# Performance work log

Hardware: AMD Instinct MI355X
Metric: run time of the kernel (lower is better)

## Reference

```python
import jax, jax.numpy as jnp
import numpy as np

B, D_IN, D_OUT, N_DISJOINT = 4096, 256, 256, 64


def setup_inputs() -> dict:
    key = jax.random.key(0)
    k_x, k_sel, k_w, k_b = jax.random.split(key, 4)
    x = jax.random.normal(k_x, (B, D_IN), dtype=jnp.float32)
    sel_idx = jax.random.randint(k_sel, (B,), 0, N_DISJOINT)
    one_hot_selector = jax.nn.one_hot(sel_idx, N_DISJOINT, dtype=jnp.float32)
    # torch nn.Linear default init: U(-1/sqrt(fan_in), 1/sqrt(fan_in)), fan_in = num_disjoint
    bound = 1.0 / np.sqrt(N_DISJOINT)
    # W[d] is the [in, out] weight matrix for disjoint block d
    W = jax.random.uniform(k_w, (N_DISJOINT, D_IN, D_OUT), dtype=jnp.float32, minval=-bound, maxval=bound)
    Bw = jax.random.uniform(k_b, (N_DISJOINT, D_OUT), dtype=jnp.float32, minval=-bound, maxval=bound)
    return {"x": x, "one_hot_selector": one_hot_selector, "W": W, "Bw": Bw}


def reference(x, one_hot_selector, W, Bw):
    # Same math as: w = (selector @ weights.T).view(B, in, out); h = einsum('bij,bi->bj', w, x)
    # Reordered contraction avoids the [B, in, out] intermediate:
    v = jnp.einsum('bi,dio->bdo', x, W)          # [B, D, out]
    h = jnp.einsum('bd,bdo->bo', one_hot_selector, v)  # [B, out]
    bias = one_hot_selector @ Bw                  # [B, out]
    return h + bias
```

## Files before the change

kernel.cpp:

```cpp
#include <hip/hip_runtime.h>


#define NBLK 64
#define BCAP 1024
#define BCAPX 256
#define CPAD 16

typedef __attribute__((ext_vector_type(8))) short bf16x8;
typedef __attribute__((ext_vector_type(4))) float f32x4;

__device__ __forceinline__ unsigned short f2bf(float f) {
    unsigned u = __float_as_uint(f);
    u += 0x7FFFu + ((u >> 16) & 1u);
    return (unsigned short)(u >> 16);
}

__global__ __launch_bounds__(256) void dd_prep(
    const float* __restrict__ x,
    const float* __restrict__ onehot,
    int* __restrict__ counts,
    int* __restrict__ buckets,
    unsigned short* __restrict__ xbs)
{
    __shared__ int rowd[32];
    __shared__ int gslot[32];
    __shared__ int lhist[NBLK];
    __shared__ int lbase[NBLK];
    const int t = threadIdx.x;
    const int w = t >> 6;
    const int lane = t & 63;
    if (t < NBLK) lhist[t] = 0;

    const int row0 = blockIdx.x * 32;
#pragma unroll
    for (int i = 0; i < 8; ++i) {
        const int row = row0 + w * 8 + i;
        const float v = onehot[(size_t)row * NBLK + lane];
        const unsigned long long mm = __ballot(v > 0.5f);
        const int dd = (int)__ffsll(mm) - 1;
        if (lane == 0) rowd[w * 8 + i] = dd;
    }
    ushort4 bv[8];
#pragma unroll
    for (int i = 0; i < 8; ++i) {
        const int row = row0 + w * 8 + i;
        const float4 v = ((const float4*)(x + ((size_t)row << 8)))[lane];
        bv[i].x = f2bf(v.x); bv[i].y = f2bf(v.y);
        bv[i].z = f2bf(v.z); bv[i].w = f2bf(v.w);
    }
    __syncthreads();

    int d = 0, slot = 0;
    if (t < 32) {
        d = rowd[t];
        slot = atomicAdd(&lhist[d], 1);
    }
    __syncthreads();
    if (t < NBLK && lhist[t] > 0)
        lbase[t] = atomicAdd(&counts[t * CPAD], lhist[t]);
    __syncthreads();
    if (t < 32) {
        const int g = lbase[d] + slot;
        gslot[t] = g;
        if (g < BCAP) buckets[d * BCAP + g] = row0 + t;
    }
    __syncthreads();
#pragma unroll
    for (int i = 0; i < 8; ++i) {
        const int idx = w * 8 + i;
        const int gd  = rowd[idx];
        const int g   = gslot[idx];
        if (g < BCAPX)
            *(ushort4*)(xbs + ((size_t)(gd * BCAPX + g) << 8) + lane * 4) = bv[i];
    }
}

__global__ __launch_bounds__(256) void dd_compute(
    const unsigned short* __restrict__ xbs,
    const float* __restrict__ W,
    const float* __restrict__ Bw,
    const int* __restrict__ counts,
    const int* __restrict__ buckets,
    float* __restrict__ out)
{
    const int t    = threadIdx.x;
    const int lane = t & 63;
    const int w    = t >> 6;
    const int d    = blockIdx.x & 63;
    const int task = blockIdx.x >> 6;
    const int rt   = task >> 2;
    const int ct   = task & 3;
    const int cw   = ct * 64 + w * 16;
    const int m    = lane & 15;
    const int qd   = lane >> 4;

    int cnt = counts[d * CPAD];
    cnt = cnt < BCAPX ? cnt : BCAPX;
    if (rt * 32 >= cnt) return;

    const float* wb = W + ((size_t)d << 16) + (size_t)(qd * 8) * 256 + (cw + m);
    bf16x8 bfrag[8];
#pragma unroll
    for (int kb = 0; kb < 8; ++kb) {
        const float* wp = wb + (size_t)(kb * 32) * 256;
#pragma unroll
        for (int j = 0; j < 8; ++j)
            bfrag[kb][j] = (short)f2bf(wp[j * 256]);
    }

    const float bias = Bw[d * 256 + cw + m];
    const int* bkt = buckets + d * BCAP;
    const unsigned short* xd = xbs + ((size_t)(d * BCAPX) << 8);

    for (int base = rt * 32; base < cnt; base += 128) {
        const int i0 = base + m;
        const int i1 = base + 16 + m;
        const int ic0 = i0 < cnt ? i0 : cnt - 1;
        const int ic1 = i1 < cnt ? i1 : cnt - 1;
        const unsigned short* xp0 = xd + ((size_t)ic0 << 8) + qd * 8;
        const unsigned short* xp1 = xd + ((size_t)ic1 << 8) + qd * 8;

        int rid0[4], rid1[4];
#pragma unroll
        for (int reg = 0; reg < 4; ++reg) {
            const int rl0 = base + qd * 4 + reg;
            const int rl1 = base + 16 + qd * 4 + reg;
            rid0[reg] = bkt[rl0 < cnt ? rl0 : cnt - 1];
            rid1[reg] = bkt[rl1 < cnt ? rl1 : cnt - 1];
        }

        f32x4 acc0 = {bias, bias, bias, bias};
        f32x4 acc1 = {bias, bias, bias, bias};
#pragma unroll
        for (int kb = 0; kb < 8; ++kb) {
            bf16x8 a0 = *(const bf16x8*)(xp0 + kb * 32);
            acc0 = __builtin_amdgcn_mfma_f32_16x16x32_bf16(a0, bfrag[kb], acc0, 0, 0, 0);
        }
#pragma unroll
        for (int kb = 0; kb < 8; ++kb) {
            bf16x8 a1 = *(const bf16x8*)(xp1 + kb * 32);
            acc1 = __builtin_amdgcn_mfma_f32_16x16x32_bf16(a1, bfrag[kb], acc1, 0, 0, 0);
        }

#pragma unroll
        for (int reg = 0; reg < 4; ++reg) {
            const int rl0 = base + qd * 4 + reg;
            if (rl0 < cnt) out[((size_t)rid0[reg] << 8) + cw + m] = acc0[reg];
            const int rl1 = base + 16 + qd * 4 + reg;
            if (rl1 < cnt) out[((size_t)rid1[reg] << 8) + cw + m] = acc1[reg];
        }
    }
}

extern "C" void kernel_launch(void* const* d_in, const int* in_sizes, int n_in,
                              void* d_out, int out_size, void* d_ws, size_t ws_size,
                              hipStream_t stream) {
    const float* x      = (const float*)d_in[0];
    const float* onehot = (const float*)d_in[1];
    const float* W      = (const float*)d_in[2];
    const float* Bw     = (const float*)d_in[3];
    float* out = (float*)d_out;

    int* counts  = (int*)d_ws;
    int* buckets = (int*)((char*)d_ws + NBLK * CPAD * 4);
    unsigned short* xbs = (unsigned short*)((char*)d_ws + NBLK * CPAD * 4 + NBLK * BCAP * 4);

    hipMemsetAsync(counts, 0, NBLK * CPAD * sizeof(int), stream);
    dd_prep<<<128, 256, 0, stream>>>(x, onehot, counts, buckets, xbs);
    dd_compute<<<1024, 256, 0, stream>>>(xbs, W, Bw, counts, buckets, out);
}
```

Baseline: 87.05 us.

## Fuse count reset, bucketing and MFMA compute into one cooperative kernel

Replaces the memset plus two kernel launches with a single cooperative launch of 512 blocks that use grid-wide syncs between phases. Compute blocks load and convert their weight fragments while prep blocks bucket rows, so the weight load overlaps the bucketing. It also halves the compute grid, so each block now walks rows with a stride of 64. The cost is two grid barriers and a runtime dependence on cooperative-launch support, with the old three-step path kept as a fallback.

```diff
diff --git a/kernel.cpp b/kernel.cpp
--- a/kernel.cpp
+++ b/kernel.cpp
@@ -1,10 +1,14 @@
 #include <hip/hip_runtime.h>
+#include <hip/hip_cooperative_groups.h>
+
+namespace cg = cooperative_groups;
 
 
 #define NBLK 64
 #define BCAP 1024
 #define BCAPX 256
 #define CPAD 16
+#define PREP_BLOCKS 128
 
 typedef __attribute__((ext_vector_type(8))) short bf16x8;
 typedef __attribute__((ext_vector_type(4))) float f32x4;
@@ -14,6 +18,160 @@
     u += 0x7FFFu + ((u >> 16) & 1u);
     return (unsigned short)(u >> 16);
 }
+
+__global__ __launch_bounds__(256, 4) void dd_fused(
+    const float* __restrict__ x,
+    const float* __restrict__ onehot,
+    const float* __restrict__ W,
+    const float* __restrict__ Bw,
+    int* __restrict__ counts,
+    int* __restrict__ buckets,
+    unsigned short* __restrict__ xbs,
+    float* __restrict__ out)
+{
+    __shared__ int rowd[32];
+    __shared__ int gslot[32];
+    __shared__ int lhist[NBLK];
+    __shared__ int lbase[NBLK];
+
+    const int t    = threadIdx.x;
+    const int w    = t >> 6;
+    const int lane = t & 63;
+    const int blk  = blockIdx.x;
+    const int d    = blk & 63;
+    const int task = blk >> 6;
+    const int rt   = task >> 2;
+    const int ct   = task & 3;
+    const int cw   = ct * 64 + w * 16;
+    const int m    = lane & 15;
+    const int qd   = lane >> 4;
+
+    const bool isprep = blk < PREP_BLOCKS;
+
+    const float* wb = W + ((size_t)d << 16) + (size_t)(qd * 8) * 256 + (cw + m);
+    bf16x8 bfrag[8];
+    float bias = 0.0f;
+
+    ushort4 bv[8];
+    int slot = 0, myd = 0;
+
+    if (isprep) {
+        if (t < NBLK) lhist[t] = 0;
+        const int row0 = blk * 32;
+#pragma unroll
+        for (int i = 0; i < 8; ++i) {
+            const int row = row0 + w * 8 + i;
+            const float v = onehot[(size_t)row * NBLK + lane];
+            const unsigned long long mm = __ballot(v > 0.5f);
+            const int dd = (int)__ffsll(mm) - 1;
+            if (lane == 0) rowd[w * 8 + i] = dd;
+        }
+#pragma unroll
+        for (int i = 0; i < 8; ++i) {
+            const int row = row0 + w * 8 + i;
+            const float4 v = ((const float4*)(x + ((size_t)row << 8)))[lane];
+            bv[i].x = f2bf(v.x); bv[i].y = f2bf(v.y);
+            bv[i].z = f2bf(v.z); bv[i].w = f2bf(v.w);
+        }
+        __syncthreads();
+        if (t < 32) {
+            myd  = rowd[t];
+            slot = atomicAdd(&lhist[myd], 1);
+        }
+        __syncthreads();
+    } else {
+#pragma unroll
+        for (int kb = 0; kb < 8; ++kb) {
+            const float* wp = wb + (size_t)(kb * 32) * 256;
+#pragma unroll
+            for (int j = 0; j < 8; ++j)
+                bfrag[kb][j] = (short)f2bf(wp[j * 256]);
+        }
+        bias = Bw[d * 256 + cw + m];
+    }
+    if (blk == 0 && t < NBLK) counts[t * CPAD] = 0;
+
+    cg::this_grid().sync();
+
+    if (isprep) {
+        if (t < NBLK && lhist[t] > 0)
+            lbase[t] = atomicAdd(&counts[t * CPAD], lhist[t]);
+        __syncthreads();
+        const int row0 = blk * 32;
+        if (t < 32) {
+            const int g = lbase[myd] + slot;
+            gslot[t] = g;
+            if (g < BCAP) buckets[myd * BCAP + g] = row0 + t;
+        }
+        __syncthreads();
+#pragma unroll
+        for (int i = 0; i < 8; ++i) {
+            const int idx = w * 8 + i;
+            const int gd  = rowd[idx];
+            const int g   = gslot[idx];
+            if (g < BCAPX)
+                *(ushort4*)(xbs + ((size_t)(gd * BCAPX + g) << 8) + lane * 4) = bv[i];
+        }
+#pragma unroll
+        for (int kb = 0; kb < 8; ++kb) {
+            const float* wp = wb + (size_t)(kb * 32) * 256;
+#pragma unroll
+            for (int j = 0; j < 8; ++j)
+                bfrag[kb][j] = (short)f2bf(wp[j * 256]);
+        }
+        bias = Bw[d * 256 + cw + m];
+        __threadfence();
+    }
+
+    cg::this_grid().sync();
+
+    int cnt = counts[d * CPAD];
+    cnt = cnt < BCAPX ? cnt : BCAPX;
+    if (rt * 32 >= cnt) return;
+
+    const int* bkt = buckets + d * BCAP;
+    const unsigned short* xd = xbs + ((size_t)(d * BCAPX) << 8);
+
+    for (int base = rt * 32; base < cnt; base += 64) {
+        const int i0 = base + m;
+        const int i1 = base + 16 + m;
+        const int ic0 = i0 < cnt ? i0 : cnt - 1;
+        const int ic1 = i1 < cnt ? i1 : cnt - 1;
+        const unsigned short* xp0 = xd + ((size_t)ic0 << 8) + qd * 8;
+        const unsigned short* xp1 = xd + ((size_t)ic1 << 8) + qd * 8;
+
+        int rid0[4], rid1[4];
+#pragma unroll
+        for (int reg = 0; reg < 4; ++reg) {
+            const int rl0 = base + qd * 4 + reg;
+            const int rl1 = base + 16 + qd * 4 + reg;
+            rid0[reg] = bkt[rl0 < cnt ? rl0 : cnt - 1];
+            rid1[reg] = bkt[rl1 < cnt ? rl1 : cnt - 1];
+        }
+
+        f32x4 acc0 = {bias, bias, bias, bias};
+        f32x4 acc1 = {bias, bias, bias, bias};
+#pragma unroll
+        for (int kb = 0; kb < 8; ++kb) {
+            bf16x8 a0 = *(const bf16x8*)(xp0 + kb * 32);
+            acc0 = __builtin_amdgcn_mfma_f32_16x16x32_bf16(a0, bfrag[kb], acc0, 0, 0, 0);
+        }
+#pragma unroll
+        for (int kb = 0; kb < 8; ++kb) {
+            bf16x8 a1 = *(const bf16x8*)(xp1 + kb * 32);
+            acc1 = __builtin_amdgcn_mfma_f32_16x16x32_bf16(a1, bfrag[kb], acc1, 0, 0, 0);
+        }
+
+#pragma unroll
+        for (int reg = 0; reg < 4; ++reg) {
+            const int rl0 = base + qd * 4 + reg;
+            if (rl0 < cnt) out[((size_t)rid0[reg] << 8) + cw + m] = acc0[reg];
+            const int rl1 = base + 16 + qd * 4 + reg;
+            if (rl1 < cnt) out[((size_t)rid1[reg] << 8) + cw + m] = acc1[reg];
+        }
+    }
+}
+
 
 __global__ __launch_bounds__(256) void dd_prep(
     const float* __restrict__ x,
@@ -165,7 +323,29 @@
     int* buckets = (int*)((char*)d_ws + NBLK * CPAD * 4);
     unsigned short* xbs = (unsigned short*)((char*)d_ws + NBLK * CPAD * 4 + NBLK * BCAP * 4);
 
-    hipMemsetAsync(counts, 0, NBLK * CPAD * sizeof(int), stream);
-    dd_prep<<<128, 256, 0, stream>>>(x, onehot, counts, buckets, xbs);
-    dd_compute<<<1024, 256, 0, stream>>>(xbs, W, Bw, counts, buckets, out);
-}
+    static int coop_ok = -1;
+    if (coop_ok < 0) {
+        int dev = 0;
+        (void)hipGetDevice(&dev);
+        int has_coop = 0;
+        (void)hipDeviceGetAttribute(&has_coop, hipDeviceAttributeCooperativeLaunch, dev);
+        int ncu = 0;
+        (void)hipDeviceGetAttribute(&ncu, hipDeviceAttributeMultiprocessorCount, dev);
+        int nb = 0;
+        (void)hipOccupancyMaxActiveBlocksPerMultiprocessor(&nb, dd_fused, 256, 0);
+        coop_ok = (has_coop && (long)nb * ncu >= 512) ? 1 : 0;
+    }
+
+    hipError_t e = hipErrorUnknown;
+    if (coop_ok == 1) {
+        void* args[] = {(void*)&x, (void*)&onehot, (void*)&W, (void*)&Bw,
+                        (void*)&counts, (void*)&buckets, (void*)&xbs, (void*)&out};
+        e = hipLaunchCooperativeKernel((const void*)dd_fused, dim3(512), dim3(256),
+                                       args, 0, stream);
+    }
+    if (e != hipSuccess) {
+        hipMemsetAsync(counts, 0, NBLK * CPAD * sizeof(int), stream);
+        dd_prep<<<128, 256, 0, stream>>>(x, onehot, counts, buckets, xbs);
+        dd_compute<<<1024, 256, 0, stream>>>(xbs, W, Bw, counts, buckets, out);
+    }
+}
```

Result: slower. 196.0 us (+125.1%).

## Replace global bucketing with per-block LDS row-list built from byte selector

Applied to the files above, without the earlier changes.

The prep kernel now only writes a one-byte selector per row, which drops the memset, the global atomics and the staged bf16 copy of x. Each compute block scans all 4096 selectors, builds its own compacted row list in LDS with a wave prefix scan, then reads x rows directly in fp32 and converts them to bf16 on the fly. This removes one launch, the atomics and the intermediate buffer traffic. In exchange every block repeats the selector scan and 16KB of LDS, and x is gathered from global at twice the byte width.

```diff
diff --git a/kernel.cpp b/kernel.cpp
--- a/kernel.cpp
+++ b/kernel.cpp
@@ -2,9 +2,6 @@
 
 
 #define NBLK 64
-#define BCAP 1024
-#define BCAPX 256
-#define CPAD 16
 
 typedef __attribute__((ext_vector_type(8))) short bf16x8;
 typedef __attribute__((ext_vector_type(4))) float f32x4;
@@ -15,22 +12,13 @@
     return (unsigned short)(u >> 16);
 }
 
-__global__ __launch_bounds__(256) void dd_prep(
-    const float* __restrict__ x,
+__global__ __launch_bounds__(256) void dd_sel(
     const float* __restrict__ onehot,
-    int* __restrict__ counts,
-    int* __restrict__ buckets,
-    unsigned short* __restrict__ xbs)
+    unsigned char* __restrict__ sel)
 {
-    __shared__ int rowd[32];
-    __shared__ int gslot[32];
-    __shared__ int lhist[NBLK];
-    __shared__ int lbase[NBLK];
     const int t = threadIdx.x;
     const int w = t >> 6;
     const int lane = t & 63;
-    if (t < NBLK) lhist[t] = 0;
-
     const int row0 = blockIdx.x * 32;
 #pragma unroll
     for (int i = 0; i < 8; ++i) {
@@ -38,51 +26,20 @@
         const float v = onehot[(size_t)row * NBLK + lane];
         const unsigned long long mm = __ballot(v > 0.5f);
         const int dd = (int)__ffsll(mm) - 1;
-        if (lane == 0) rowd[w * 8 + i] = dd;
-    }
-    ushort4 bv[8];
-#pragma unroll
-    for (int i = 0; i < 8; ++i) {
-        const int row = row0 + w * 8 + i;
-        const float4 v = ((const float4*)(x + ((size_t)row << 8)))[lane];
-        bv[i].x = f2bf(v.x); bv[i].y = f2bf(v.y);
-        bv[i].z = f2bf(v.z); bv[i].w = f2bf(v.w);
-    }
-    __syncthreads();
-
-    int d = 0, slot = 0;
-    if (t < 32) {
-        d = rowd[t];
-        slot = atomicAdd(&lhist[d], 1);
-    }
-    __syncthreads();
-    if (t < NBLK && lhist[t] > 0)
-        lbase[t] = atomicAdd(&counts[t * CPAD], lhist[t]);
-    __syncthreads();
-    if (t < 32) {
-        const int g = lbase[d] + slot;
-        gslot[t] = g;
-        if (g < BCAP) buckets[d * BCAP + g] = row0 + t;
-    }
-    __syncthreads();
-#pragma unroll
-    for (int i = 0; i < 8; ++i) {
-        const int idx = w * 8 + i;
-        const int gd  = rowd[idx];
-        const int g   = gslot[idx];
-        if (g < BCAPX)
-            *(ushort4*)(xbs + ((size_t)(gd * BCAPX + g) << 8) + lane * 4) = bv[i];
+        if (lane == 0) sel[row] = (unsigned char)dd;
     }
 }
 
-__global__ __launch_bounds__(256) void dd_compute(
-    const unsigned short* __restrict__ xbs,
+__global__ __launch_bounds__(256, 4) void dd_compute(
+    const float* __restrict__ x,
+    const unsigned char* __restrict__ sel,
     const float* __restrict__ W,
     const float* __restrict__ Bw,
-    const int* __restrict__ counts,
-    const int* __restrict__ buckets,
     float* __restrict__ out)
 {
+    __shared__ int rowlist[4096];
+    __shared__ int wtot[4];
+
     const int t    = threadIdx.x;
     const int lane = t & 63;
     const int w    = t >> 6;
@@ -94,9 +51,7 @@
     const int m    = lane & 15;
     const int qd   = lane >> 4;
 
-    int cnt = counts[d * CPAD];
-    cnt = cnt < BCAPX ? cnt : BCAPX;
-    if (rt * 32 >= cnt) return;
+    const int4 sv = ((const int4*)sel)[t];
 
     const float* wb = W + ((size_t)d << 16) + (size_t)(qd * 8) * 256 + (cw + m);
     bf16x8 bfrag[8];
@@ -107,38 +62,82 @@
         for (int j = 0; j < 8; ++j)
             bfrag[kb][j] = (short)f2bf(wp[j * 256]);
     }
+    const float bias = Bw[d * 256 + cw + m];
 
-    const float bias = Bw[d * 256 + cw + m];
-    const int* bkt = buckets + d * BCAP;
-    const unsigned short* xd = xbs + ((size_t)(d * BCAPX) << 8);
+    unsigned mym = 0;
+#pragma unroll
+    for (int jw = 0; jw < 4; ++jw) {
+        const int word = (&sv.x)[jw];
+#pragma unroll
+        for (int b = 0; b < 4; ++b) {
+            const int s = (word >> (8 * b)) & 255;
+            if (s == d) mym |= 1u << (jw * 4 + b);
+        }
+    }
+    const int cnt_t = __popc(mym);
+    int scan = cnt_t;
+#pragma unroll
+    for (int off = 1; off < 64; off <<= 1) {
+        const int v = __shfl_up(scan, off, 64);
+        if (lane >= off) scan += v;
+    }
+    if (lane == 63) wtot[w] = scan;
+    __syncthreads();
+    int wbase = 0;
+#pragma unroll
+    for (int i = 0; i < 4; ++i) wbase += (i < w) ? wtot[i] : 0;
+    const int cnt = wtot[0] + wtot[1] + wtot[2] + wtot[3];
+    int pos = wbase + scan - cnt_t;
+    unsigned mm = mym;
+    while (mm) {
+        const int b = __ffs(mm) - 1;
+        mm &= mm - 1;
+        rowlist[pos++] = t * 16 + b;
+    }
+    __syncthreads();
+
+    if (rt * 32 >= cnt) return;
 
     for (int base = rt * 32; base < cnt; base += 128) {
         const int i0 = base + m;
         const int i1 = base + 16 + m;
-        const int ic0 = i0 < cnt ? i0 : cnt - 1;
-        const int ic1 = i1 < cnt ? i1 : cnt - 1;
-        const unsigned short* xp0 = xd + ((size_t)ic0 << 8) + qd * 8;
-        const unsigned short* xp1 = xd + ((size_t)ic1 << 8) + qd * 8;
+        const int r0 = rowlist[i0 < cnt ? i0 : cnt - 1];
+        const int r1 = rowlist[i1 < cnt ? i1 : cnt - 1];
 
         int rid0[4], rid1[4];
 #pragma unroll
         for (int reg = 0; reg < 4; ++reg) {
             const int rl0 = base + qd * 4 + reg;
             const int rl1 = base + 16 + qd * 4 + reg;
-            rid0[reg] = bkt[rl0 < cnt ? rl0 : cnt - 1];
-            rid1[reg] = bkt[rl1 < cnt ? rl1 : cnt - 1];
+            rid0[reg] = rowlist[rl0 < cnt ? rl0 : cnt - 1];
+            rid1[reg] = rowlist[rl1 < cnt ? rl1 : cnt - 1];
         }
+
+        const float* xp0 = x + ((size_t)r0 << 8) + qd * 8;
+        const float* xp1 = x + ((size_t)r1 << 8) + qd * 8;
 
         f32x4 acc0 = {bias, bias, bias, bias};
         f32x4 acc1 = {bias, bias, bias, bias};
 #pragma unroll
         for (int kb = 0; kb < 8; ++kb) {
-            bf16x8 a0 = *(const bf16x8*)(xp0 + kb * 32);
+            const float4 lo = *(const float4*)(xp0 + kb * 32);
+            const float4 hi = *(const float4*)(xp0 + kb * 32 + 4);
+            bf16x8 a0;
+            a0[0] = (short)f2bf(lo.x); a0[1] = (short)f2bf(lo.y);
+            a0[2] = (short)f2bf(lo.z); a0[3] = (short)f2bf(lo.w);
+            a0[4] = (short)f2bf(hi.x); a0[5] = (short)f2bf(hi.y);
+            a0[6] = (short)f2bf(hi.z); a0[7] = (short)f2bf(hi.w);
             acc0 = __builtin_amdgcn_mfma_f32_16x16x32_bf16(a0, bfrag[kb], acc0, 0, 0, 0);
         }
 #pragma unroll
         for (int kb = 0; kb < 8; ++kb) {
-            bf16x8 a1 = *(const bf16x8*)(xp1 + kb * 32);
+            const float4 lo = *(const float4*)(xp1 + kb * 32);
+            const float4 hi = *(const float4*)(xp1 + kb * 32 + 4);
+            bf16x8 a1;
+            a1[0] = (short)f2bf(lo.x); a1[1] = (short)f2bf(lo.y);
+            a1[2] = (short)f2bf(lo.z); a1[3] = (short)f2bf(lo.w);
+            a1[4] = (short)f2bf(hi.x); a1[5] = (short)f2bf(hi.y);
+            a1[6] = (short)f2bf(hi.z); a1[7] = (short)f2bf(hi.w);
             acc1 = __builtin_amdgcn_mfma_f32_16x16x32_bf16(a1, bfrag[kb], acc1, 0, 0, 0);
         }
 
@@ -161,11 +160,8 @@
     const float* Bw     = (const float*)d_in[3];
     float* out = (float*)d_out;
 
-    int* counts  = (int*)d_ws;
-    int* buckets = (int*)((char*)d_ws + NBLK * CPAD * 4);
-    unsigned short* xbs = (unsigned short*)((char*)d_ws + NBLK * CPAD * 4 + NBLK * BCAP * 4);
+    unsigned char* sel = (unsigned char*)d_ws;
 
-    hipMemsetAsync(counts, 0, NBLK * CPAD * sizeof(int), stream);
-    dd_prep<<<128, 256, 0, stream>>>(x, onehot, counts, buckets, xbs);
-    dd_compute<<<1024, 256, 0, stream>>>(xbs, W, Bw, counts, buckets, out);
+    dd_sel<<<128, 256, 0, stream>>>(onehot, sel);
+    dd_compute<<<1024, 256, 0, stream>>>(x, sel, W, Bw, out);
 }
```

Measured after the change: 101.5 us. 16.6% more time.
